# Optimization experiments

Measured on AMD Instinct MI355X. Metric: run time of the kernel, lower is better.

Reference implementation:

```python
import jax, jax.numpy as jnp
import numpy as np

NUM_WORDS = 10000
IN_DIM = 300
SIZE = 256
NUM_SEQ = 2
B = 16
L = 128
NUM_BASE_LEMMAS = 3000


def _lstm(x, Wi, Wh, b):
    # x: [L, B, D] -> hidden states [L, B, H]
    Bb = x.shape[1]
    H = Wh.shape[0]
    def step(carry, xt):
        h, c = carry
        z = xt @ Wi + h @ Wh + b  # [B, 4H], gate order i,f,g,o (torch convention)
        i, f, g, o = jnp.split(z, 4, axis=-1)
        c = jax.nn.sigmoid(f) * c + jax.nn.sigmoid(i) * jnp.tanh(g)
        h = jax.nn.sigmoid(o) * jnp.tanh(c)
        return (h, c), h
    init = (jnp.zeros((Bb, H), x.dtype), jnp.zeros((Bb, H), x.dtype))
    _, hs = jax.lax.scan(step, init, x)
    return hs


def _bilstm(x, lengths, Wi_f, Wh_f, b_f, Wi_b, Wh_b, b_b):
    # x: [B, L, D]; variable-length bidirectional LSTM, concat outputs [B, L, 2H]
    Bb, Ll, _ = x.shape
    t = jnp.arange(Ll)
    # reverse the valid prefix of each row; padding stays in place
    rev_idx = jnp.where(t[None, :] < lengths[:, None], lengths[:, None] - 1 - t[None, :], t[None, :])
    x_rev = jnp.take_along_axis(x, rev_idx[:, :, None], axis=1)
    hf = _lstm(jnp.swapaxes(x, 0, 1), Wi_f, Wh_f, b_f)
    hb = _lstm(jnp.swapaxes(x_rev, 0, 1), Wi_b, Wh_b, b_b)
    hf = jnp.swapaxes(hf, 0, 1)
    hb = jnp.take_along_axis(jnp.swapaxes(hb, 0, 1), rev_idx[:, :, None], axis=1)
    return jnp.concatenate([hf, hb], axis=-1)


def setup_inputs() -> dict:
    key = jax.random.key(0)
    ks = jax.random.split(key, 16)
    d = {}
    d['word_embeddings'] = jax.random.normal(ks[0], (NUM_WORDS, IN_DIM), jnp.float32)
    # embedding projection Linear(IN_DIM, SIZE)
    d['Wp'] = jax.random.normal(ks[1], (IN_DIM, SIZE), jnp.float32) * 0.05
    d['bp'] = jnp.zeros((SIZE,), jnp.float32)
    D = SIZE + NUM_SEQ
    d['Wi_f'] = jax.random.normal(ks[2], (D, 4 * SIZE), jnp.float32) * 0.05
    d['Wh_f'] = jax.random.normal(ks[3], (SIZE, 4 * SIZE), jnp.float32) * 0.05
    d['b_f'] = jnp.zeros((4 * SIZE,), jnp.float32)
    d['Wi_b'] = jax.random.normal(ks[4], (D, 4 * SIZE), jnp.float32) * 0.05
    d['Wh_b'] = jax.random.normal(ks[5], (SIZE, 4 * SIZE), jnp.float32) * 0.05
    d['b_b'] = jnp.zeros((4 * SIZE,), jnp.float32)
    # encoded projection Linear(2*SIZE, SIZE)
    d['Wenc'] = jax.random.normal(ks[6], (2 * SIZE, SIZE), jnp.float32) * 0.05
    d['benc'] = jnp.zeros((SIZE,), jnp.float32)
    # gate projection Linear(2*SIZE, SIZE), bias init 1.0 per source
    d['Wgate'] = jax.random.normal(ks[7], (2 * SIZE, SIZE), jnp.float32) * 0.05
    d['bgate'] = jnp.ones((SIZE,), jnp.float32)
    d['seq0'] = jax.random.randint(ks[8], (B, L), 0, NUM_WORDS, jnp.int32)
    d['seq1'] = jax.random.randint(ks[9], (B, L), 0, NUM_WORDS, jnp.int32)
    d['len0'] = jax.random.randint(ks[10], (B,), 1, L + 1, jnp.int32)
    d['len1'] = jax.random.randint(ks[11], (B,), 1, L + 1, jnp.int32)
    d['u2l'] = jax.random.randint(ks[12], (NUM_WORDS,), 0, NUM_BASE_LEMMAS, jnp.int32)
    return d


def reference(word_embeddings, Wp, bp, Wi_f, Wh_f, b_f, Wi_b, Wh_b, b_b, Wenc, benc, Wgate, bgate, seq0, seq1, len0, len1, u2l):
    num_words = word_embeddings.shape[0]
    batch = seq0.shape[0]
    size = Wp.shape[1]
    we = jax.nn.relu(word_embeddings @ Wp + bp)  # [num_words, size]
    offsets = jnp.arange(batch, dtype=jnp.int32) * num_words  # [B]
    u2l_off = (u2l[None, :] + offsets[:, None]).reshape(-1)  # [B*num_words]
    num_lemmas = batch * num_words
    ctxt = jnp.tile(we, (batch, 1))  # [B*num_words, size]
    for i, (seq, lengths) in enumerate(((seq0, len0), (seq1, len1))):
        Ll = seq.shape[1]
        seq_off = seq + offsets[:, None]  # [B, L]
        enc_in = ctxt[seq_off]  # gather: [B, L, size]
        mode = jnp.zeros((batch, Ll, NUM_SEQ), enc_in.dtype).at[:, :, i].set(1.0)
        enc_in = jnp.concatenate([enc_in, mode], axis=-1)  # [B, L, size+num_seq]
        h = _bilstm(enc_in, lengths, Wi_f, Wh_f, b_f, Wi_b, Wh_b, b_b)  # [B, L, 2*size]
        enc = h @ Wenc + benc  # [B, L, size]
        mask = (jnp.arange(Ll)[None, :] < lengths[:, None]).astype(enc.dtype)
        enc = enc * mask[:, :, None]
        seq_lemmas = u2l_off[seq_off.reshape(-1)]  # [B*L]
        new_lemma = jax.ops.segment_max(enc.reshape(-1, size), seq_lemmas, num_segments=num_lemmas)
        new_lemma = jax.nn.relu(new_lemma)  # empty segments (-inf) -> 0
        new_word = new_lemma[u2l_off]  # scatter-back via gather: [B*num_words, size]
        gate = jax.nn.sigmoid(jnp.concatenate([ctxt, new_word], axis=-1) @ Wgate + bgate)
        ctxt = ctxt * gate + (1.0 - gate) * new_word
    return ctxt
```

## Files before the change

kernel.cpp:

```cpp
#include <hip/hip_runtime.h>

#define NW    10000
#define INDIM 300
#define SZ    256
#define BB    16
#define LL    128
#define NLEM  3000
#define FH    1024
#define NCAP  8192

typedef short  bf16x8 __attribute__((ext_vector_type(8)));
typedef float  f32x4  __attribute__((ext_vector_type(4)));

__device__ __forceinline__ float sigf(float x){
  return __builtin_amdgcn_rcpf(1.f+__builtin_amdgcn_exp2f(-1.442695041f*x));
}
__device__ __forceinline__ float tanhf_(float x){
  return fmaf(-2.f, __builtin_amdgcn_rcpf(1.f+__builtin_amdgcn_exp2f(2.885390082f*x)), 1.f);
}
__device__ __forceinline__ short f2b(float f){
  unsigned u=__float_as_uint(f); u += 0x7FFFu + ((u>>16)&1u); return (short)(u>>16);
}
#define B2F(s) __uint_as_float(((unsigned)(unsigned short)(s))<<16)

__global__ void k_we(const float* __restrict__ emb, const float* __restrict__ Wp,
                     const float* __restrict__ bp, float* __restrict__ we){
  __shared__ __align__(16) float As[16][INDIM];
  int r0 = blockIdx.x*16, tid = threadIdx.x;
  for(int i=tid;i<16*INDIM;i+=256){int lr=i/INDIM,d=i-lr*INDIM;
    As[lr][d]=emb[(long)(r0+lr)*INDIM+d];}
  __syncthreads();
  int cl=tid&63, rg=tid>>6;
  float acc[4][4];
  #pragma unroll
  for(int i=0;i<4;i++){acc[i][0]=acc[i][1]=acc[i][2]=acc[i][3]=0.f;}
  for(int k=0;k<INDIM;k+=4){
    float4 a4[4];
    #pragma unroll
    for(int i=0;i<4;i++) a4[i]=*(const float4*)&As[rg*4+i][k];
    #pragma unroll
    for(int j=0;j<4;j++){
      const float* wr=Wp+(long)(k+j)*SZ+cl;
      float w0=wr[0],w1=wr[64],w2=wr[128],w3=wr[192];
      #pragma unroll
      for(int i=0;i<4;i++){
        float a=(j==0)?a4[i].x:(j==1)?a4[i].y:(j==2)?a4[i].z:a4[i].w;
        acc[i][0]=fmaf(a,w0,acc[i][0]);acc[i][1]=fmaf(a,w1,acc[i][1]);
        acc[i][2]=fmaf(a,w2,acc[i][2]);acc[i][3]=fmaf(a,w3,acc[i][3]);
      }
    }
  }
  #pragma unroll
  for(int i=0;i<4;i++){
    int r=r0+rg*4+i;
    #pragma unroll
    for(int cc=0;cc<4;cc++){int col=cl+cc*64;
      we[(long)r*SZ+col]=fmaxf(acc[i][cc]+bp[col],0.f);}
  }
}

__global__ void k_xwi(const int* __restrict__ seq, const int* __restrict__ len,
                      const float* __restrict__ srcw, long bstride,
                      const float* __restrict__ ctxtT, const int* __restrict__ idxmap,
                      const float* __restrict__ Wi_f, const float* __restrict__ bvf,
                      const float* __restrict__ Wi_b, const float* __restrict__ bvb,
                      int iseq, short* __restrict__ xwo){
  __shared__ __align__(16) float As[64][SZ];
  __shared__ const float* rowp[64];
  int r0=blockIdx.x*64, cb=blockIdx.y, tid=threadIdx.x;
  int dir=r0>>11;
  if(tid<64){
    int grow=r0+tid;
    int t=(grow>>4)&(LL-1), b=grow&(BB-1);
    int lb=len[b];
    int tt=(dir==0)? t : ((t<lb)? (lb-1-t) : t);
    int tok=seq[b*LL+tt];
    const float* rp;
    if(idxmap){
      int im=idxmap[b*NW+tok];
      rp = (im>=0)? ctxtT+(long)im*SZ : srcw+(long)tok*SZ;
    }else{
      rp = srcw + (long)b*bstride + (long)tok*SZ;
    }
    rowp[tid]=rp;
  }
  __syncthreads();
  for(int i=tid;i<64*SZ;i+=256){int lr=i>>8,j=i&(SZ-1);As[lr][j]=rowp[lr][j];}
  __syncthreads();
  const float* __restrict__ Wi = dir? Wi_b : Wi_f;
  const float* __restrict__ bv = dir? bvb : bvf;
  int cl=tid&63, rg=tid>>6, c0=cb*256+cl;
  float acc[16][4];
  #pragma unroll
  for(int i=0;i<16;i++){acc[i][0]=acc[i][1]=acc[i][2]=acc[i][3]=0.f;}
  for(int k=0;k<SZ;k+=4){
    float4 a4[16];
    #pragma unroll
    for(int i=0;i<16;i++) a4[i]=*(const float4*)&As[rg*16+i][k];
    #pragma unroll
    for(int j=0;j<4;j++){
      const float* wr=Wi+(long)(k+j)*FH+c0;
      float w0=wr[0],w1=wr[64],w2=wr[128],w3=wr[192];
      #pragma unroll
      for(int i=0;i<16;i++){
        float a=(j==0)?a4[i].x:(j==1)?a4[i].y:(j==2)?a4[i].z:a4[i].w;
        acc[i][0]=fmaf(a,w0,acc[i][0]);acc[i][1]=fmaf(a,w1,acc[i][1]);
        acc[i][2]=fmaf(a,w2,acc[i][2]);acc[i][3]=fmaf(a,w3,acc[i][3]);
      }
    }
  }
  #pragma unroll
  for(int cc=0;cc<4;cc++){
    int cx=c0+cc*64;
    float be=Wi[(long)(SZ+iseq)*FH+cx]+bv[cx];
    int g=cx>>8, unit=cx&255, w2=unit>>5, s2=(unit>>4)&1, nl=unit&15;
    #pragma unroll
    for(int i=0;i<16;i++){
      int grow=r0+rg*16+i;
      int b=grow&15, t=(grow>>4)&127, d2=grow>>11;
      long sidx=((((long)d2*128+t)*8 + w2)*64 + (b>>2)*16+nl)*32 + s2*16 + g*4 + (b&3);
      xwo[sidx]=f2b(acc[i][cc]+be);
    }
  }
}

__global__ void k_prep(const float* __restrict__ Wh_f, const float* __restrict__ Wh_b,
                       short* __restrict__ frag){
  int tid = blockIdx.x*256 + threadIdx.x;
  int l=tid&63, f=(tid>>6)&63, w=(tid>>12)&7, dir=tid>>15;
  const float* Wh = dir? Wh_b : Wh_f;
  int ks=f&7, T2=f>>3, s2=T2>>2, g=T2&3;
  int col = g*256 + w*32 + s2*16 + (l&15);
  int k0  = ks*32 + (l>>4)*8;
  short v[8];
  #pragma unroll
  for(int j=0;j<8;j++) v[j]=f2b(Wh[(long)(k0+j)*FH + col]);
  *(bf16x8*)(frag + (long)tid*8) = *(bf16x8*)v;
}

#define MFA(a,b,c) __builtin_amdgcn_mfma_f32_16x16x32_bf16(a,b,c,0,0,0)
#define LDFW(f)    (*(const bf16x8*)(fr + (long)(f)*512 + l*8))
#define LDLW(i2,ks) (*(const bf16x8*)(bl + ((i2)*8+(ks))*512 + l*8))
#define DECLWT(T) bf16x8 W##T##_0=LDFW((T)*8+0),W##T##_1=LDFW((T)*8+1),W##T##_2=LDFW((T)*8+2),W##T##_3=LDFW((T)*8+3),W##T##_4=LDFW((T)*8+4),W##T##_5=LDFW((T)*8+5),W##T##_6=LDFW((T)*8+6),W##T##_7=LDFW((T)*8+7);
#define MMRT(T,Cv) { Cv=MFA(A0,W##T##_0,Cv); Cv=MFA(A1,W##T##_1,Cv); Cv=MFA(A2,W##T##_2,Cv); Cv=MFA(A3,W##T##_3,Cv); Cv=MFA(A4,W##T##_4,Cv); Cv=MFA(A5,W##T##_5,Cv); Cv=MFA(A6,W##T##_6,Cv); Cv=MFA(A7,W##T##_7,Cv); }
#define MMLT(i2,Cv) { Cv=MFA(A0,LDLW(i2,0),Cv); Cv=MFA(A1,LDLW(i2,1),Cv); Cv=MFA(A2,LDLW(i2,2),Cv); Cv=MFA(A3,LDLW(i2,3),Cv); Cv=MFA(A4,LDLW(i2,4),Cv); Cv=MFA(A5,LDLW(i2,5),Cv); Cv=MFA(A6,LDLW(i2,6),Cv); Cv=MFA(A7,LDLW(i2,7),Cv); }
#define MMST(Cv) { Cv=MFA(A0,S0,Cv); Cv=MFA(A1,S1,Cv); Cv=MFA(A2,S2,Cv); Cv=MFA(A3,S3,Cv); Cv=MFA(A4,S4,Cv); Cv=MFA(A5,S5,Cv); Cv=MFA(A6,S6,Cv); Cv=MFA(A7,S7,Cv); }
#define LOADST(f0) S0=LDFW((f0)+0); S1=LDFW((f0)+1); S2=LDFW((f0)+2); S3=LDFW((f0)+3); S4=LDFW((f0)+4); S5=LDFW((f0)+5); S6=LDFW((f0)+6); S7=LDFW((f0)+7);
#define G1(s,r,CA,CB,CC,CD,XA,XB) { \
  float zi=CA[r]+B2F(XA[r]), zf=CB[r]+B2F(XA[4+(r)]), zg=CC[r]+B2F(XB[r]), zo=CD[r]+B2F(XB[4+(r)]); \
  cst_##s##_##r = sigf(zf)*cst_##s##_##r + sigf(zi)*tanhf_(zg); \
  float hv = sigf(zo)*tanhf_(cst_##s##_##r); \
  int b_=4*(l>>4)+(r); int u_=w*32+(s)*16+(l&15); \
  hbn[b_*264+u_]=f2b(hv); }
#define GP(s,CA,CB,CC,CD,XA,XB) \
  G1(s,0,CA,CB,CC,CD,XA,XB) G1(s,1,CA,CB,CC,CD,XA,XB) \
  G1(s,2,CA,CB,CC,CD,XA,XB) G1(s,3,CA,CB,CC,CD,XA,XB)

extern __shared__ char smem_raw[];

__global__ __launch_bounds__(512,2) void k_lstm_w8(
    const short* __restrict__ frag, const short* __restrict__ xq,
    short* __restrict__ hgs){
  const int dir=blockIdx.x, tid=threadIdx.x, w=tid>>6, l=tid&63;
  short* hb=(short*)smem_raw;
  short* bl=(short*)(smem_raw+16896)+w*8192;
  const short* fr = frag + (long)(dir*8+w)*32768;
  for(int i=tid;i<4224;i+=512) ((int*)smem_raw)[i]=0;
  #pragma unroll
  for(int c2=0;c2<16;c2++)
    *(f32x4*)(bl+c2*512+l*8) = *(const f32x4*)(fr+(long)(32+c2)*512+l*8);
  DECLWT(0) DECLWT(1) DECLWT(2) DECLWT(3)
  float cst_0_0=0,cst_0_1=0,cst_0_2=0,cst_0_3=0,
        cst_1_0=0,cst_1_1=0,cst_1_2=0,cst_1_3=0;
  __syncthreads();
  const short* xwb = xq + ((long)dir*128*8 + w)*2048 + (long)l*32;
  short* hgb = hgs + (long)dir*524288;
  const int db=tid>>5, du=(tid&31)*8;
  bf16x8 S0,S1,S2,S3,S4,S5,S6,S7;
  for(int t=0;t<LL;t++){
    const int cur=t&1, nxt=cur^1;
    LOADST(48)
    const short* xp = xwb + (long)t*16384;
    bf16x8 X0=*(const bf16x8*)(xp+0), X1=*(const bf16x8*)(xp+8);
    const short* hr = hb + cur*4224 + (l&15)*264 + (l>>4)*8;
    bf16x8 A0=*(const bf16x8*)(hr+0),   A1=*(const bf16x8*)(hr+32),
           A2=*(const bf16x8*)(hr+64),  A3=*(const bf16x8*)(hr+96),
           A4=*(const bf16x8*)(hr+128), A5=*(const bf16x8*)(hr+160),
           A6=*(const bf16x8*)(hr+192), A7=*(const bf16x8*)(hr+224);
    f32x4 Z={0.f,0.f,0.f,0.f};
    f32x4 C00=Z,C01=Z,C02=Z,C03=Z,C10=Z,C11=Z,C12=Z,C13=Z;
    MMRT(0,C00) MMRT(1,C01) MMRT(2,C02) MMRT(3,C03)
    MMLT(0,C10) MMLT(1,C11)
    MMST(C12)
    LOADST(56)
    bf16x8 X2=*(const bf16x8*)(xp+16), X3=*(const bf16x8*)(xp+24);
    short* hbn = hb + nxt*4224;
    GP(0, C00,C01,C02,C03, X0,X1)
    MMST(C13)
    GP(1, C10,C11,C12,C13, X2,X3)
    __syncthreads();
    f32x4 hv4 = *(const f32x4*)(hbn + db*264 + du);
    *(f32x4*)(hgb + ((long)t*16 + db)*256 + du) = hv4;
  }
}

__global__ void k_enc(const int* __restrict__ seq, const int* __restrict__ len,
                      const int* __restrict__ u2l, const short* __restrict__ hgs,
                      const float* __restrict__ Wenc, const float* __restrict__ benc,
                      unsigned int* __restrict__ lembuf, unsigned int* __restrict__ flags){
  __shared__ __align__(16) float As[16][2*SZ];
  __shared__ const short* pf16[16]; __shared__ const short* pb16[16];
  __shared__ int lem_s[16], val_s[16], b_s[16];
  int r0=blockIdx.x*16, tid=threadIdx.x;
  if(tid<16){
    int r=r0+tid, b=r>>7, t=r&127, lb=len[b];
    int v=(t<lb); val_s[tid]=v; b_s[tid]=b;
    int lem=u2l[seq[r]];
    lem_s[tid]=lem;
    pf16[tid]=hgs+((long)t*BB+b)*SZ;
    int tr=v? (lb-1-t) : t;
    pb16[tid]=hgs+((long)(LL+tr)*BB+b)*SZ;
    if(v) flags[(long)b*NLEM+lem]=1u;
  }
  __syncthreads();
  for(int i=tid;i<16*SZ;i+=256){int lr=i>>8,j=i&(SZ-1);
    As[lr][j]=B2F(pf16[lr][j]); As[lr][SZ+j]=B2F(pb16[lr][j]);}
  __syncthreads();
  int cl=tid&63, rg=tid>>6;
  float acc[4][4];
  #pragma unroll
  for(int i=0;i<4;i++){acc[i][0]=acc[i][1]=acc[i][2]=acc[i][3]=0.f;}
  for(int k=0;k<2*SZ;k+=4){
    float4 a4[4];
    #pragma unroll
    for(int i=0;i<4;i++) a4[i]=*(const float4*)&As[rg*4+i][k];
    #pragma unroll
    for(int j=0;j<4;j++){
      const float* wr=Wenc+(long)(k+j)*SZ+cl;
      float w0=wr[0],w1=wr[64],w2=wr[128],w3=wr[192];
      #pragma unroll
      for(int i=0;i<4;i++){
        float a=(j==0)?a4[i].x:(j==1)?a4[i].y:(j==2)?a4[i].z:a4[i].w;
        acc[i][0]=fmaf(a,w0,acc[i][0]);acc[i][1]=fmaf(a,w1,acc[i][1]);
        acc[i][2]=fmaf(a,w2,acc[i][2]);acc[i][3]=fmaf(a,w3,acc[i][3]);
      }
    }
  }
  #pragma unroll
  for(int i=0;i<4;i++){
    int lr=rg*4+i;
    if(val_s[lr]){
      long base=((long)b_s[lr]*NLEM+lem_s[lr])*SZ;
      #pragma unroll
      for(int cc=0;cc<4;cc++){
        int col=cl+cc*64;
        float e=fmaxf(acc[i][cc]+benc[col],0.f);
        atomicMax(&lembuf[base+col], __float_as_uint(e));
      }
    }
  }
}

__global__ void k_rowgemm(const float* __restrict__ A, const float* __restrict__ W,
                          float* __restrict__ C, const unsigned int* __restrict__ flags){
  __shared__ __align__(16) float As[16][SZ];
  __shared__ int any_s;
  int r0=blockIdx.x*16, tid=threadIdx.x;
  if(tid==0){
    int a = flags? 0 : 1;
    if(flags){ for(int i=0;i<16;i++) a |= (int)flags[r0+i]; }
    any_s=a;
  }
  __syncthreads();
  if(!any_s) return;
  for(int i=tid;i<16*SZ;i+=256){int lr=i>>8,j=i&(SZ-1);As[lr][j]=A[(long)(r0+lr)*SZ+j];}
  __syncthreads();
  int cl=tid&63, rg=tid>>6;
  float acc[4][4];
  #pragma unroll
  for(int i=0;i<4;i++){acc[i][0]=acc[i][1]=acc[i][2]=acc[i][3]=0.f;}
  for(int k=0;k<SZ;k+=4){
    float4 a4[4];
    #pragma unroll
    for(int i=0;i<4;i++) a4[i]=*(const float4*)&As[rg*4+i][k];
    #pragma unroll
    for(int j=0;j<4;j++){
      const float* wr=W+(long)(k+j)*SZ+cl;
      float w0=wr[0],w1=wr[64],w2=wr[128],w3=wr[192];
      #pragma unroll
      for(int i=0;i<4;i++){
        float a=(j==0)?a4[i].x:(j==1)?a4[i].y:(j==2)?a4[i].z:a4[i].w;
        acc[i][0]=fmaf(a,w0,acc[i][0]);acc[i][1]=fmaf(a,w1,acc[i][1]);
        acc[i][2]=fmaf(a,w2,acc[i][2]);acc[i][3]=fmaf(a,w3,acc[i][3]);
      }
    }
  }
  #pragma unroll
  for(int i=0;i<4;i++){
    int r=r0+rg*4+i;
    #pragma unroll
    for(int cc=0;cc<4;cc++) C[(long)r*SZ+cl+cc*64]=acc[i][cc];
  }
}

__global__ void k_rowgemm_n(const float* __restrict__ A, const float* __restrict__ W,
                            float* __restrict__ C, const int* __restrict__ cnt, int ncap){
  __shared__ __align__(16) float As[16][SZ];
  int n=*cnt; if(n>ncap)n=ncap;
  int r0=blockIdx.x*16, tid=threadIdx.x;
  if(r0>=n) return;
  for(int i=tid;i<16*SZ;i+=256){int lr=i>>8,j=i&(SZ-1);
    As[lr][j]= (r0+lr<n)? A[(long)(r0+lr)*SZ+j] : 0.f;}
  __syncthreads();
  int cl=tid&63, rg=tid>>6;
  float acc[4][4];
  #pragma unroll
  for(int i=0;i<4;i++){acc[i][0]=acc[i][1]=acc[i][2]=acc[i][3]=0.f;}
  for(int k=0;k<SZ;k+=4){
    float4 a4[4];
    #pragma unroll
    for(int i=0;i<4;i++) a4[i]=*(const float4*)&As[rg*4+i][k];
    #pragma unroll
    for(int j=0;j<4;j++){
      const float* wr=W+(long)(k+j)*SZ+cl;
      float w0=wr[0],w1=wr[64],w2=wr[128],w3=wr[192];
      #pragma unroll
      for(int i=0;i<4;i++){
        float a=(j==0)?a4[i].x:(j==1)?a4[i].y:(j==2)?a4[i].z:a4[i].w;
        acc[i][0]=fmaf(a,w0,acc[i][0]);acc[i][1]=fmaf(a,w1,acc[i][1]);
        acc[i][2]=fmaf(a,w2,acc[i][2]);acc[i][3]=fmaf(a,w3,acc[i][3]);
      }
    }
  }
  #pragma unroll
  for(int i=0;i<4;i++){
    int r=r0+rg*4+i;
    if(r<n){
      #pragma unroll
      for(int cc=0;cc<4;cc++) C[(long)r*SZ+cl+cc*64]=acc[i][cc];
    }
  }
}

__global__ void k_compact(const int* __restrict__ u2l, const unsigned int* __restrict__ flags,
                          int* __restrict__ cnt, int* __restrict__ list,
                          int* __restrict__ idxmap, int ncap){
  int r = blockIdx.x*256+threadIdx.x;
  if(r>=BB*NW) return;
  int b=r/NW, w=r-b*NW;
  int im=-1;
  if(flags[(long)b*NLEM+u2l[w]]){
    int idx=atomicAdd(cnt,1);
    if(idx<ncap){ list[idx]=r; im=idx; }
  }
  idxmap[r]=im;
}

__global__ void k_gate0c(const float* __restrict__ we, const float* __restrict__ P0,
                         const float* __restrict__ Q, const float* __restrict__ lembuf,
                         const int* __restrict__ u2l, const float* __restrict__ bg,
                         const int* __restrict__ cnt, const int* __restrict__ list,
                         float* __restrict__ ctxtT, int ncap){
  int n=*cnt; if(n>ncap)n=ncap;
  long idx=(long)blockIdx.x*256+threadIdx.x;
  long i=idx>>6; int k4=(int)(idx&63);
  if(i>=n) return;
  int r=list[i]; int b=r/NW, w=r-b*NW;
  int lem=u2l[w];
  long qb=((long)b*NLEM+lem)*SZ;
  float4 p =((const float4*)(P0+(long)w*SZ))[k4];
  float4 wv=((const float4*)(we+(long)w*SZ))[k4];
  float4 bgv=((const float4*)bg)[k4];
  float4 q =((const float4*)(Q+qb))[k4];
  float4 nw=((const float4*)(lembuf+qb))[k4];
  float4 o;
  { float g=sigf(p.x+q.x+bgv.x); o.x=wv.x*g+(1.f-g)*nw.x; }
  { float g=sigf(p.y+q.y+bgv.y); o.y=wv.y*g+(1.f-g)*nw.y; }
  { float g=sigf(p.z+q.z+bgv.z); o.z=wv.z*g+(1.f-g)*nw.z; }
  { float g=sigf(p.w+q.w+bgv.w); o.w=wv.w*g+(1.f-g)*nw.w; }
  ((float4*)ctxtT)[i*64+k4]=o;
}

__global__ void k_base0ip(float* __restrict__ we, const float* __restrict__ P0,
                          const float* __restrict__ bg){
  long idx=(long)blockIdx.x*256+threadIdx.x;
  if(idx>=(long)NW*SZ/4) return;
  int k4=(int)(idx&63);
  float4 wv=((float4*)we)[idx];
  float4 p =((const float4*)P0)[idx];
  float4 bgv=((const float4*)bg)[k4];
  wv.x*=sigf(p.x+bgv.x); wv.y*=sigf(p.y+bgv.y);
  wv.z*=sigf(p.z+bgv.z); wv.w*=sigf(p.w+bgv.w);
  ((float4*)we)[idx]=wv;
}

__global__ void k_gate0(const float* __restrict__ we, const float* __restrict__ P0,
                        const float* __restrict__ Q, const float* __restrict__ lembuf,
                        const int* __restrict__ u2l, const unsigned int* __restrict__ flags,
                        const float* __restrict__ bg, float* __restrict__ out){
  long idx=(long)blockIdx.x*256+threadIdx.x;
  const long TOTAL4=(long)BB*NW*SZ/4;
  if(idx>=TOTAL4) return;
  long row=idx>>6; int k4=(int)(idx&63);
  int r32=(int)row;
  int b=r32/NW, w=r32-b*NW;
  int lem=u2l[w];
  long qb=((long)b*NLEM+lem)*SZ;
  unsigned int fl=flags[(long)b*NLEM+lem];
  float4 p =((const float4*)(P0+(long)w*SZ))[k4];
  float4 wv=((const float4*)(we+(long)w*SZ))[k4];
  float4 bgv=((const float4*)bg)[k4];
  float4 q, nw;
  if(fl){ q=((const float4*)(Q+qb))[k4]; nw=((const float4*)(lembuf+qb))[k4]; }
  else  { q=make_float4(0.f,0.f,0.f,0.f); nw=q; }
  float4 o;
  { float g=sigf(p.x+q.x+bgv.x); o.x=wv.x*g+(1.f-g)*nw.x; }
  { float g=sigf(p.y+q.y+bgv.y); o.y=wv.y*g+(1.f-g)*nw.y; }
  { float g=sigf(p.z+q.z+bgv.z); o.z=wv.z*g+(1.f-g)*nw.z; }
  { float g=sigf(p.w+q.w+bgv.w); o.w=wv.w*g+(1.f-g)*nw.w; }
  ((float4*)out)[idx]=o;
}

__global__ void k_gate1e(const float* __restrict__ base0, const float* __restrict__ ctxtT,
                         const float* __restrict__ P1b, const float* __restrict__ Pt,
                         const int* __restrict__ idxmap,
                         const float* __restrict__ Q, const float* __restrict__ lembuf,
                         const int* __restrict__ u2l, const unsigned int* __restrict__ flags,
                         const float* __restrict__ bg, float* __restrict__ out){
  long idx=(long)blockIdx.x*256+threadIdx.x;
  const long TOTAL4=(long)BB*NW*SZ/4;
  if(idx>=TOTAL4) return;
  long row=idx>>6; int k4=(int)(idx&63);
  int r32=(int)row;
  int b=r32/NW, w=r32-b*NW;
  int im=idxmap[r32];
  int lem=u2l[w];
  long qb=((long)b*NLEM+lem)*SZ;
  unsigned int fl=flags[(long)b*NLEM+lem];
  float4 p, cv;
  if(im>=0){ p=((const float4*)(Pt+(long)im*SZ))[k4]; cv=((const float4*)(ctxtT+(long)im*SZ))[k4]; }
  else     { p=((const float4*)(P1b+(long)w*SZ))[k4]; cv=((const float4*)(base0+(long)w*SZ))[k4]; }
  float4 bgv=((const float4*)bg)[k4];
  float4 q, nw;
  if(fl){ q=((const float4*)(Q+qb))[k4]; nw=((const float4*)(lembuf+qb))[k4]; }
  else  { q=make_float4(0.f,0.f,0.f,0.f); nw=q; }
  float4 o;
  { float g=sigf(p.x+q.x+bgv.x); o.x=cv.x*g+(1.f-g)*nw.x; }
  { float g=sigf(p.y+q.y+bgv.y); o.y=cv.y*g+(1.f-g)*nw.y; }
  { float g=sigf(p.z+q.z+bgv.z); o.z=cv.z*g+(1.f-g)*nw.z; }
  { float g=sigf(p.w+q.w+bgv.w); o.w=cv.w*g+(1.f-g)*nw.w; }
  ((float4*)out)[idx]=o;
}

__global__ void k_gate1(const float* __restrict__ ctxt, const float* __restrict__ Wg,
                        const float* __restrict__ Q, const float* __restrict__ lembuf,
                        const int* __restrict__ u2l, const unsigned int* __restrict__ flags,
                        const float* __restrict__ bg, float* __restrict__ out){
  __shared__ __align__(16) float As[64][SZ];
  __shared__ __align__(16) float Ws[64][SZ];
  __shared__ int lem_s[64];
  int r0=blockIdx.x*64, tid=threadIdx.x;
  for(int i=tid;i<64*SZ;i+=256){int lr=i>>8,j=i&(SZ-1);
    As[lr][j]=ctxt[(long)(r0+lr)*SZ+j];}
  if(tid<64){int r=r0+tid; lem_s[tid]=u2l[r%NW];}
  int cl=tid&63, rg=tid>>6;
  float acc[16][4];
  #pragma unroll
  for(int i=0;i<16;i++){acc[i][0]=acc[i][1]=acc[i][2]=acc[i][3]=0.f;}
  for(int kb=0;kb<4;kb++){
    __syncthreads();
    for(int i=tid;i<64*SZ;i+=256){int lr=i>>8,j=i&(SZ-1);
      Ws[lr][j]=Wg[(long)(kb*64+lr)*SZ+j];}
    __syncthreads();
    for(int k=0;k<64;k+=4){
      float4 a4[16];
      #pragma unroll
      for(int i=0;i<16;i++) a4[i]=*(const float4*)&As[rg*16+i][kb*64+k];
      #pragma unroll
      for(int j=0;j<4;j++){
        float w0=Ws[k+j][cl],w1=Ws[k+j][cl+64],w2=Ws[k+j][cl+128],w3=Ws[k+j][cl+192];
        #pragma unroll
        for(int i=0;i<16;i++){
          float a=(j==0)?a4[i].x:(j==1)?a4[i].y:(j==2)?a4[i].z:a4[i].w;
          acc[i][0]=fmaf(a,w0,acc[i][0]);acc[i][1]=fmaf(a,w1,acc[i][1]);
          acc[i][2]=fmaf(a,w2,acc[i][2]);acc[i][3]=fmaf(a,w3,acc[i][3]);
        }
      }
    }
  }
  #pragma unroll
  for(int i=0;i<16;i++){
    int lr=rg*16+i, r=r0+lr, b=r/NW;
    long base=((long)b*NLEM+lem_s[lr])*SZ;
    unsigned int fl=flags[(long)b*NLEM+lem_s[lr]];
    #pragma unroll
    for(int cc=0;cc<4;cc++){
      int col=cl+cc*64;
      float qv=0.f, nw=0.f;
      if(fl){ qv=Q[base+col]; nw=lembuf[base+col]; }
      float g=sigf(acc[i][cc]+qv+bg[col]);
      out[(long)r*SZ+col]=As[lr][col]*g+(1.f-g)*nw;
    }
  }
}

extern "C" void kernel_launch(void* const* d_in, const int* in_sizes, int n_in,
                              void* d_out, int out_size, void* d_ws, size_t ws_size,
                              hipStream_t stream){
  const float* emb  =(const float*)d_in[0];
  const float* Wp   =(const float*)d_in[1];
  const float* bp   =(const float*)d_in[2];
  const float* Wi_f =(const float*)d_in[3];
  const float* Wh_f =(const float*)d_in[4];
  const float* b_f  =(const float*)d_in[5];
  const float* Wi_b =(const float*)d_in[6];
  const float* Wh_b =(const float*)d_in[7];
  const float* b_b  =(const float*)d_in[8];
  const float* Wenc =(const float*)d_in[9];
  const float* benc =(const float*)d_in[10];
  const float* Wg   =(const float*)d_in[11];
  const float* bg   =(const float*)d_in[12];
  const int*   seq0 =(const int*)d_in[13];
  const int*   seq1 =(const int*)d_in[14];
  const int*   len0 =(const int*)d_in[15];
  const int*   len1 =(const int*)d_in[16];
  const int*   u2l  =(const int*)d_in[17];

  float* ws    = (float*)d_ws;
  float* we    = ws;
  float* xwi   = we    + 2560000;
  float* ctxtT = xwi   + 2097152;
  float* hglob = xwi   + 4194304;
  float* lembuf= hglob + 1048576;
  float* flags = lembuf+ 12288000;
  float* Q     = flags + 48000;
  float* P0    = Q     + 12288000;
  short* whb   = (short*)(P0 + 2560000);
  int*   idxmap= (int*)(P0 + 2560000 + 262144);
  int*   list  = idxmap + 160000;
  int*   cnt   = list + NCAP;
  float* Ptouch= (float*)(cnt + 4);
  long base_floats = (long)(Ptouch - ws);
  long avail = ((long)(ws_size/4) - base_floats)/SZ;
  int sparse_ok = (avail >= NCAP);
  float* out   = (float*)d_out;

  hipFuncSetAttribute((const void*)k_lstm_w8,
                      hipFuncAttributeMaxDynamicSharedMemorySize, 147968);

  k_we<<<NW/16,256,0,stream>>>(emb,Wp,bp,we);
  k_rowgemm<<<NW/16,256,0,stream>>>(we,Wg,P0,nullptr);
  k_prep<<<256,256,0,stream>>>(Wh_f,Wh_b,whb);

  hipMemsetAsync(lembuf,0,(size_t)(12288000+48000)*4,stream);
  dim3 gx(64,4);
  k_xwi<<<gx,256,0,stream>>>(seq0,len0,we,0L,nullptr,nullptr,
                             Wi_f,b_f,Wi_b,b_b,0,(short*)xwi);
  k_lstm_w8<<<2,512,147968,stream>>>(whb,(const short*)xwi,(short*)hglob);
  k_enc<<<BB*LL/16,256,0,stream>>>(seq0,len0,u2l,(const short*)hglob,Wenc,benc,
                                   (unsigned int*)lembuf,(unsigned int*)flags);
  k_rowgemm<<<BB*NLEM/16,256,0,stream>>>(lembuf,Wg+(long)SZ*SZ,Q,
                                         (const unsigned int*)flags);
  if(sparse_ok){
    hipMemsetAsync(cnt,0,4,stream);
    k_compact<<<(BB*NW+255)/256,256,0,stream>>>(u2l,(const unsigned int*)flags,
                                                cnt,list,idxmap,NCAP);
    k_gate0c<<<NCAP*64/256,256,0,stream>>>(we,P0,Q,lembuf,u2l,bg,cnt,list,ctxtT,NCAP);
    k_rowgemm_n<<<NCAP/16,256,0,stream>>>(ctxtT,Wg,Ptouch,cnt,NCAP);
    k_base0ip<<<(NW*SZ/4+255)/256,256,0,stream>>>(we,P0,bg);
    k_rowgemm<<<NW/16,256,0,stream>>>(we,Wg,P0,nullptr);
  }else{
    long nb=((long)BB*NW*SZ/4+255)/256;
    k_gate0<<<(int)nb,256,0,stream>>>(we,P0,Q,lembuf,u2l,
                                      (const unsigned int*)flags,bg,out);
  }

  hipMemsetAsync(lembuf,0,(size_t)(12288000+48000)*4,stream);
  if(sparse_ok){
    k_xwi<<<gx,256,0,stream>>>(seq1,len1,we,0L,ctxtT,idxmap,
                               Wi_f,b_f,Wi_b,b_b,1,(short*)xwi);
  }else{
    k_xwi<<<gx,256,0,stream>>>(seq1,len1,out,(long)NW*SZ,nullptr,nullptr,
                               Wi_f,b_f,Wi_b,b_b,1,(short*)xwi);
  }
  k_lstm_w8<<<2,512,147968,stream>>>(whb,(const short*)xwi,(short*)hglob);
  k_enc<<<BB*LL/16,256,0,stream>>>(seq1,len1,u2l,(const short*)hglob,Wenc,benc,
                                   (unsigned int*)lembuf,(unsigned int*)flags);
  k_rowgemm<<<BB*NLEM/16,256,0,stream>>>(lembuf,Wg+(long)SZ*SZ,Q,
                                         (const unsigned int*)flags);
  if(sparse_ok){
    long nb=((long)BB*NW*SZ/4+255)/256;
    k_gate1e<<<(int)nb,256,0,stream>>>(we,ctxtT,P0,Ptouch,idxmap,Q,lembuf,u2l,
                                       (const unsigned int*)flags,bg,out);
  }else{
    k_gate1<<<BB*NW/64,256,0,stream>>>(out,Wg,Q,lembuf,u2l,
                                       (const unsigned int*)flags,bg,out);
  }
}
```

Baseline: 1.392 ms.

## Move input-projection and encoder GEMMs to bf16 MFMA with prepacked weight fragments

Replaces the FP32 scalar-FMA GEMMs in the LSTM input-projection and encoder kernels with bf16 MFMA kernels. Weights are prepacked once into fragment layout, and activation tiles are staged in shared memory as bf16. The encoder also handles 64 rows per block instead of 16. It adds s_setprio around the MFMA sections of the recurrent LSTM loop to favour matrix issue. The cost is lower precision in these GEMMs, though the outputs were already stored as bf16, plus extra prep kernels and workspace; the xwi grid also shrinks to 64 blocks, which may underfill the GPU.

```diff
diff --git a/kernel.cpp b/kernel.cpp
--- a/kernel.cpp
+++ b/kernel.cpp
@@ -21,7 +21,11 @@
 __device__ __forceinline__ short f2b(float f){
   unsigned u=__float_as_uint(f); u += 0x7FFFu + ((u>>16)&1u); return (short)(u>>16);
 }
+__device__ __forceinline__ int pack2(float a, float b){
+  return ((int)(unsigned short)f2b(a)) | (((int)(unsigned short)f2b(b))<<16);
+}
 #define B2F(s) __uint_as_float(((unsigned)(unsigned short)(s))<<16)
+#define MFA(a,b,c) __builtin_amdgcn_mfma_f32_16x16x32_bf16(a,b,c,0,0,0)
 
 __global__ void k_we(const float* __restrict__ emb, const float* __restrict__ Wp,
                      const float* __restrict__ bp, float* __restrict__ we){
@@ -59,19 +63,56 @@
   }
 }
 
-__global__ void k_xwi(const int* __restrict__ seq, const int* __restrict__ len,
+__global__ void k_prep(const float* __restrict__ Wh_f, const float* __restrict__ Wh_b,
+                       short* __restrict__ frag){
+  int tid = blockIdx.x*256 + threadIdx.x;
+  int l=tid&63, f=(tid>>6)&63, w=(tid>>12)&7, dir=tid>>15;
+  const float* Wh = dir? Wh_b : Wh_f;
+  int ks=f&7, T2=f>>3, s2=T2>>2, g=T2&3;
+  int col = g*256 + w*32 + s2*16 + (l&15);
+  int k0  = ks*32 + (l>>4)*8;
+  short v[8];
+  #pragma unroll
+  for(int j=0;j<8;j++) v[j]=f2b(Wh[(long)(k0+j)*FH + col]);
+  *(bf16x8*)(frag + (long)tid*8) = *(bf16x8*)v;
+}
+
+__global__ void k_prepwi(const float* __restrict__ Wi_f, const float* __restrict__ Wi_b,
+                         short* __restrict__ wf){
+  int tid = blockIdx.x*256 + threadIdx.x;
+  int l=tid&63, ks=(tid>>6)&7, ct=(tid>>9)&63, dir=tid>>15;
+  const float* Wi = dir? Wi_b : Wi_f;
+  int col = ct*16 + (l&15);
+  int k0  = ks*32 + (l>>4)*8;
+  short v[8];
+  #pragma unroll
+  for(int j=0;j<8;j++) v[j]=f2b(Wi[(long)(k0+j)*FH + col]);
+  *(bf16x8*)(wf + (long)tid*8) = *(bf16x8*)v;
+}
+
+__global__ void k_prepenc(const float* __restrict__ Wenc, short* __restrict__ wef){
+  int tid = blockIdx.x*256 + threadIdx.x;
+  int l=tid&63, ks=(tid>>6)&15, ct=tid>>10;
+  int col = ct*16 + (l&15);
+  int k0  = ks*32 + (l>>4)*8;
+  short v[8];
+  #pragma unroll
+  for(int j=0;j<8;j++) v[j]=f2b(Wenc[(long)(k0+j)*SZ + col]);
+  *(bf16x8*)(wef + (long)tid*8) = *(bf16x8*)v;
+}
+
+__global__ void k_xwi_mfma(const int* __restrict__ seq, const int* __restrict__ len,
                       const float* __restrict__ srcw, long bstride,
                       const float* __restrict__ ctxtT, const int* __restrict__ idxmap,
                       const float* __restrict__ Wi_f, const float* __restrict__ bvf,
                       const float* __restrict__ Wi_b, const float* __restrict__ bvb,
-                      int iseq, short* __restrict__ xwo){
-  __shared__ __align__(16) float As[64][SZ];
+                      const short* __restrict__ wf, int iseq, short* __restrict__ xwo){
+  __shared__ __align__(16) short As[64*264];
   __shared__ const float* rowp[64];
-  int r0=blockIdx.x*64, cb=blockIdx.y, tid=threadIdx.x;
-  int dir=r0>>11;
+  int bx=blockIdx.x, dir=bx>>5, blk=bx&31, tid=threadIdx.x;
+  int w=tid>>6, l=tid&63;
   if(tid<64){
-    int grow=r0+tid;
-    int t=(grow>>4)&(LL-1), b=grow&(BB-1);
+    int t = blk*4 + (tid>>4), b = tid&15;
     int lb=len[b];
     int tt=(dir==0)? t : ((t<lb)? (lb-1-t) : t);
     int tok=seq[b*LL+tt];
@@ -85,60 +126,45 @@
     rowp[tid]=rp;
   }
   __syncthreads();
-  for(int i=tid;i<64*SZ;i+=256){int lr=i>>8,j=i&(SZ-1);As[lr][j]=rowp[lr][j];}
+  for(int i2=tid;i2<64*64;i2+=256){
+    int lr=i2>>6, c4=(i2&63)*4;
+    float4 v=*(const float4*)(rowp[lr]+c4);
+    int2 pk; pk.x=pack2(v.x,v.y); pk.y=pack2(v.z,v.w);
+    *(int2*)&As[lr*264+c4]=pk;
+  }
   __syncthreads();
   const float* __restrict__ Wi = dir? Wi_b : Wi_f;
   const float* __restrict__ bv = dir? bvb : bvf;
-  int cl=tid&63, rg=tid>>6, c0=cb*256+cl;
-  float acc[16][4];
-  #pragma unroll
-  for(int i=0;i<16;i++){acc[i][0]=acc[i][1]=acc[i][2]=acc[i][3]=0.f;}
-  for(int k=0;k<SZ;k+=4){
-    float4 a4[16];
-    #pragma unroll
-    for(int i=0;i<16;i++) a4[i]=*(const float4*)&As[rg*16+i][k];
-    #pragma unroll
-    for(int j=0;j<4;j++){
-      const float* wr=Wi+(long)(k+j)*FH+c0;
-      float w0=wr[0],w1=wr[64],w2=wr[128],w3=wr[192];
-      #pragma unroll
-      for(int i=0;i<16;i++){
-        float a=(j==0)?a4[i].x:(j==1)?a4[i].y:(j==2)?a4[i].z:a4[i].w;
-        acc[i][0]=fmaf(a,w0,acc[i][0]);acc[i][1]=fmaf(a,w1,acc[i][1]);
-        acc[i][2]=fmaf(a,w2,acc[i][2]);acc[i][3]=fmaf(a,w3,acc[i][3]);
-      }
-    }
-  }
-  #pragma unroll
-  for(int cc=0;cc<4;cc++){
-    int cx=c0+cc*64;
-    float be=Wi[(long)(SZ+iseq)*FH+cx]+bv[cx];
-    int g=cx>>8, unit=cx&255, w2=unit>>5, s2=(unit>>4)&1, nl=unit&15;
-    #pragma unroll
-    for(int i=0;i<16;i++){
-      int grow=r0+rg*16+i;
-      int b=grow&15, t=(grow>>4)&127, d2=grow>>11;
-      long sidx=((((long)d2*128+t)*8 + w2)*64 + (b>>2)*16+nl)*32 + s2*16 + g*4 + (b&3);
-      xwo[sidx]=f2b(acc[i][cc]+be);
-    }
-  }
-}
-
-__global__ void k_prep(const float* __restrict__ Wh_f, const float* __restrict__ Wh_b,
-                       short* __restrict__ frag){
-  int tid = blockIdx.x*256 + threadIdx.x;
-  int l=tid&63, f=(tid>>6)&63, w=(tid>>12)&7, dir=tid>>15;
-  const float* Wh = dir? Wh_b : Wh_f;
-  int ks=f&7, T2=f>>3, s2=T2>>2, g=T2&3;
-  int col = g*256 + w*32 + s2*16 + (l&15);
-  int k0  = ks*32 + (l>>4)*8;
-  short v[8];
-  #pragma unroll
-  for(int j=0;j<8;j++) v[j]=f2b(Wh[(long)(k0+j)*FH + col]);
-  *(bf16x8*)(frag + (long)tid*8) = *(bf16x8*)v;
-}
-
-#define MFA(a,b,c) __builtin_amdgcn_mfma_f32_16x16x32_bf16(a,b,c,0,0,0)
+  const short* wfd = wf + (long)dir*262144;
+  for(int n2=0;n2<16;n2++){
+    int ct = w*16 + n2;
+    const short* bfp = wfd + ((long)ct*8)*512 + l*8;
+    f32x4 Z={0.f,0.f,0.f,0.f};
+    f32x4 C0=Z,C1=Z,C2=Z,C3=Z;
+    #pragma unroll
+    for(int ks=0;ks<8;ks++){
+      bf16x8 bb=*(const bf16x8*)(bfp + ks*512);
+      int ao = ks*32 + (l>>4)*8;
+      bf16x8 a0=*(const bf16x8*)(&As[((l&15)    )*264 + ao]);
+      bf16x8 a1=*(const bf16x8*)(&As[((l&15)+16 )*264 + ao]);
+      bf16x8 a2=*(const bf16x8*)(&As[((l&15)+32 )*264 + ao]);
+      bf16x8 a3=*(const bf16x8*)(&As[((l&15)+48 )*264 + ao]);
+      C0=MFA(a0,bb,C0); C1=MFA(a1,bb,C1); C2=MFA(a2,bb,C2); C3=MFA(a3,bb,C3);
+    }
+    int g=ct>>4, w2=(ct&15)>>1, s2=ct&1;
+    int col = g*256 + w2*32 + s2*16 + (l&15);
+    float be = Wi[(long)(SZ+iseq)*FH+col] + bv[col];
+    #pragma unroll
+    for(int m=0;m<4;m++){
+      f32x4 Cm = (m==0)?C0:(m==1)?C1:(m==2)?C2:C3;
+      long base=((((long)dir*128 + blk*4 + m)*8 + w2)*64 + (l>>4)*16 + (l&15))*32
+                + s2*16 + g*4;
+      int2 pk; pk.x=pack2(Cm[0]+be,Cm[1]+be); pk.y=pack2(Cm[2]+be,Cm[3]+be);
+      *(int2*)(xwo+base)=pk;
+    }
+  }
+}
+
 #define LDFW(f)    (*(const bf16x8*)(fr + (long)(f)*512 + l*8))
 #define LDLW(i2,ks) (*(const bf16x8*)(bl + ((i2)*8+(ks))*512 + l*8))
 #define DECLWT(T) bf16x8 W##T##_0=LDFW((T)*8+0),W##T##_1=LDFW((T)*8+1),W##T##_2=LDFW((T)*8+2),W##T##_3=LDFW((T)*8+3),W##T##_4=LDFW((T)*8+4),W##T##_5=LDFW((T)*8+5),W##T##_6=LDFW((T)*8+6),W##T##_7=LDFW((T)*8+7);
@@ -189,14 +215,18 @@
            A6=*(const bf16x8*)(hr+192), A7=*(const bf16x8*)(hr+224);
     f32x4 Z={0.f,0.f,0.f,0.f};
     f32x4 C00=Z,C01=Z,C02=Z,C03=Z,C10=Z,C11=Z,C12=Z,C13=Z;
+    __builtin_amdgcn_s_setprio(1);
     MMRT(0,C00) MMRT(1,C01) MMRT(2,C02) MMRT(3,C03)
     MMLT(0,C10) MMLT(1,C11)
     MMST(C12)
+    __builtin_amdgcn_s_setprio(0);
     LOADST(56)
     bf16x8 X2=*(const bf16x8*)(xp+16), X3=*(const bf16x8*)(xp+24);
     short* hbn = hb + nxt*4224;
     GP(0, C00,C01,C02,C03, X0,X1)
+    __builtin_amdgcn_s_setprio(1);
     MMST(C13)
+    __builtin_amdgcn_s_setprio(0);
     GP(1, C10,C11,C12,C13, X2,X3)
     __syncthreads();
     f32x4 hv4 = *(const f32x4*)(hbn + db*264 + du);
@@ -204,58 +234,56 @@
   }
 }
 
-__global__ void k_enc(const int* __restrict__ seq, const int* __restrict__ len,
+__global__ void k_enc_mfma(const int* __restrict__ seq, const int* __restrict__ len,
                       const int* __restrict__ u2l, const short* __restrict__ hgs,
-                      const float* __restrict__ Wenc, const float* __restrict__ benc,
+                      const short* __restrict__ wef, const float* __restrict__ benc,
                       unsigned int* __restrict__ lembuf, unsigned int* __restrict__ flags){
-  __shared__ __align__(16) float As[16][2*SZ];
-  __shared__ const short* pf16[16]; __shared__ const short* pb16[16];
-  __shared__ int lem_s[16], val_s[16], b_s[16];
-  int r0=blockIdx.x*16, tid=threadIdx.x;
-  if(tid<16){
+  __shared__ __align__(16) short As[64*520];
+  __shared__ const short* pf16[64]; __shared__ const short* pb16[64];
+  __shared__ int lem_s[64], val_s[64], b_s[64];
+  int r0=blockIdx.x*64, tid=threadIdx.x, w=tid>>6, l=tid&63;
+  if(tid<64){
     int r=r0+tid, b=r>>7, t=r&127, lb=len[b];
     int v=(t<lb); val_s[tid]=v; b_s[tid]=b;
-    int lem=u2l[seq[r]];
-    lem_s[tid]=lem;
+    int lem=u2l[seq[r]]; lem_s[tid]=lem;
     pf16[tid]=hgs+((long)t*BB+b)*SZ;
     int tr=v? (lb-1-t) : t;
     pb16[tid]=hgs+((long)(LL+tr)*BB+b)*SZ;
     if(v) flags[(long)b*NLEM+lem]=1u;
   }
   __syncthreads();
-  for(int i=tid;i<16*SZ;i+=256){int lr=i>>8,j=i&(SZ-1);
-    As[lr][j]=B2F(pf16[lr][j]); As[lr][SZ+j]=B2F(pb16[lr][j]);}
-  __syncthreads();
-  int cl=tid&63, rg=tid>>6;
-  float acc[4][4];
-  #pragma unroll
-  for(int i=0;i<4;i++){acc[i][0]=acc[i][1]=acc[i][2]=acc[i][3]=0.f;}
-  for(int k=0;k<2*SZ;k+=4){
-    float4 a4[4];
-    #pragma unroll
-    for(int i=0;i<4;i++) a4[i]=*(const float4*)&As[rg*4+i][k];
-    #pragma unroll
-    for(int j=0;j<4;j++){
-      const float* wr=Wenc+(long)(k+j)*SZ+cl;
-      float w0=wr[0],w1=wr[64],w2=wr[128],w3=wr[192];
+  for(int i2=tid;i2<64*128;i2+=256){
+    int lr=i2>>7, cc=(i2&127)*4;
+    const short* sp=(cc<256)? pf16[lr]+cc : pb16[lr]+(cc-256);
+    *(int2*)&As[lr*520+cc]=*(const int2*)sp;
+  }
+  __syncthreads();
+  for(int n2=0;n2<4;n2++){
+    int ct=w*4+n2;
+    f32x4 Z={0.f,0.f,0.f,0.f};
+    f32x4 C0=Z,C1=Z,C2=Z,C3=Z;
+    #pragma unroll
+    for(int ks=0;ks<16;ks++){
+      bf16x8 bb=*(const bf16x8*)(wef+((long)(ct*16+ks))*512+l*8);
+      int ao=ks*32+(l>>4)*8;
+      bf16x8 a0=*(const bf16x8*)(&As[((l&15)    )*520+ao]);
+      bf16x8 a1=*(const bf16x8*)(&As[((l&15)+16 )*520+ao]);
+      bf16x8 a2=*(const bf16x8*)(&As[((l&15)+32 )*520+ao]);
+      bf16x8 a3=*(const bf16x8*)(&As[((l&15)+48 )*520+ao]);
+      C0=MFA(a0,bb,C0); C1=MFA(a1,bb,C1); C2=MFA(a2,bb,C2); C3=MFA(a3,bb,C3);
+    }
+    int col=ct*16+(l&15);
+    float be=benc[col];
+    #pragma unroll
+    for(int m=0;m<4;m++){
+      f32x4 Cm=(m==0)?C0:(m==1)?C1:(m==2)?C2:C3;
       #pragma unroll
-      for(int i=0;i<4;i++){
-        float a=(j==0)?a4[i].x:(j==1)?a4[i].y:(j==2)?a4[i].z:a4[i].w;
-        acc[i][0]=fmaf(a,w0,acc[i][0]);acc[i][1]=fmaf(a,w1,acc[i][1]);
-        acc[i][2]=fmaf(a,w2,acc[i][2]);acc[i][3]=fmaf(a,w3,acc[i][3]);
-      }
-    }
-  }
-  #pragma unroll
-  for(int i=0;i<4;i++){
-    int lr=rg*4+i;
-    if(val_s[lr]){
-      long base=((long)b_s[lr]*NLEM+lem_s[lr])*SZ;
-      #pragma unroll
-      for(int cc=0;cc<4;cc++){
-        int col=cl+cc*64;
-        float e=fmaxf(acc[i][cc]+benc[col],0.f);
-        atomicMax(&lembuf[base+col], __float_as_uint(e));
+      for(int reg=0;reg<4;reg++){
+        int row=m*16+(l>>4)*4+reg;
+        if(val_s[row]){
+          float e=fmaxf(Cm[reg]+be,0.f);
+          atomicMax(&lembuf[((long)b_s[row]*NLEM+lem_s[row])*SZ+col], __float_as_uint(e));
+        }
       }
     }
   }
@@ -536,7 +564,9 @@
   float* Q     = flags + 48000;
   float* P0    = Q     + 12288000;
   short* whb   = (short*)(P0 + 2560000);
-  int*   idxmap= (int*)(P0 + 2560000 + 262144);
+  short* wifrag= whb + 524288;
+  short* wefrag= wifrag + 524288;
+  int*   idxmap= (int*)(P0 + 2560000 + 262144 + 262144 + 65536);
   int*   list  = idxmap + 160000;
   int*   cnt   = list + NCAP;
   float* Ptouch= (float*)(cnt + 4);
@@ -551,14 +581,15 @@
   k_we<<<NW/16,256,0,stream>>>(emb,Wp,bp,we);
   k_rowgemm<<<NW/16,256,0,stream>>>(we,Wg,P0,nullptr);
   k_prep<<<256,256,0,stream>>>(Wh_f,Wh_b,whb);
+  k_prepwi<<<256,256,0,stream>>>(Wi_f,Wi_b,wifrag);
+  k_prepenc<<<64,256,0,stream>>>(Wenc,wefrag);
 
   hipMemsetAsync(lembuf,0,(size_t)(12288000+48000)*4,stream);
-  dim3 gx(64,4);
-  k_xwi<<<gx,256,0,stream>>>(seq0,len0,we,0L,nullptr,nullptr,
-                             Wi_f,b_f,Wi_b,b_b,0,(short*)xwi);
+  k_xwi_mfma<<<64,256,0,stream>>>(seq0,len0,we,0L,nullptr,nullptr,
+                                  Wi_f,b_f,Wi_b,b_b,wifrag,0,(short*)xwi);
   k_lstm_w8<<<2,512,147968,stream>>>(whb,(const short*)xwi,(short*)hglob);
-  k_enc<<<BB*LL/16,256,0,stream>>>(seq0,len0,u2l,(const short*)hglob,Wenc,benc,
-                                   (unsigned int*)lembuf,(unsigned int*)flags);
+  k_enc_mfma<<<BB*LL/64,256,0,stream>>>(seq0,len0,u2l,(const short*)hglob,wefrag,benc,
+                                        (unsigned int*)lembuf,(unsigned int*)flags);
   k_rowgemm<<<BB*NLEM/16,256,0,stream>>>(lembuf,Wg+(long)SZ*SZ,Q,
                                          (const unsigned int*)flags);
   if(sparse_ok){
@@ -577,15 +608,15 @@
 
   hipMemsetAsync(lembuf,0,(size_t)(12288000+48000)*4,stream);
   if(sparse_ok){
-    k_xwi<<<gx,256,0,stream>>>(seq1,len1,we,0L,ctxtT,idxmap,
-                               Wi_f,b_f,Wi_b,b_b,1,(short*)xwi);
+    k_xwi_mfma<<<64,256,0,stream>>>(seq1,len1,we,0L,ctxtT,idxmap,
+                                    Wi_f,b_f,Wi_b,b_b,wifrag,1,(short*)xwi);
   }else{
-    k_xwi<<<gx,256,0,stream>>>(seq1,len1,out,(long)NW*SZ,nullptr,nullptr,
-                               Wi_f,b_f,Wi_b,b_b,1,(short*)xwi);
+    k_xwi_mfma<<<64,256,0,stream>>>(seq1,len1,out,(long)NW*SZ,nullptr,nullptr,
+                                    Wi_f,b_f,Wi_b,b_b,wifrag,1,(short*)xwi);
   }
   k_lstm_w8<<<2,512,147968,stream>>>(whb,(const short*)xwi,(short*)hglob);
-  k_enc<<<BB*LL/16,256,0,stream>>>(seq1,len1,u2l,(const short*)hglob,Wenc,benc,
-                                   (unsigned int*)lembuf,(unsigned int*)flags);
+  k_enc_mfma<<<BB*LL/64,256,0,stream>>>(seq1,len1,u2l,(const short*)hglob,wefrag,benc,
+                                        (unsigned int*)lembuf,(unsigned int*)flags);
   k_rowgemm<<<BB*NLEM/16,256,0,stream>>>(lembuf,Wg+(long)SZ*SZ,Q,
                                          (const unsigned int*)flags);
   if(sparse_ok){
```

After: 1.585 ms. +13.9%, slower.
